# Performance work log

Hardware: AMD Instinct MI355X
Metric: run time of the kernel (lower is better)

The kernel has to match this reference:

```python
import jax, jax.numpy as jnp
import numpy as np

N_NODES = 100000
N_EDGES = 1600000
D = 64
K = 5


def setup_inputs() -> dict:
    key = jax.random.key(0)
    k1, k2, k3, k4 = jax.random.split(key, 4)
    x = jax.random.normal(k1, (N_NODES, D), dtype=jnp.float32)
    # random edges, guaranteed no self-loops (offset in [1, N-1])
    src = jax.random.randint(k2, (N_EDGES,), 0, N_NODES)
    off = jax.random.randint(k3, (N_EDGES,), 1, N_NODES)
    dst = (src + off) % N_NODES
    edge_index = jnp.stack([src, dst], axis=0)  # [2, E], row 0 = source j, row 1 = target i
    kW, kb = jax.random.split(k4)
    W = jax.random.normal(kW, (K, D, D), dtype=jnp.float32) * (1.0 / np.sqrt(D))
    b = jnp.zeros((D,), dtype=jnp.float32)
    return {"x": x, "edge_index": edge_index, "W": W, "b": b}


def reference(x, edge_index, W, b):
    """ChebConv (normalization='sym', lambda_max=2.0) as in PyG GnBlock.

    Scaled Laplacian L_hat = (2/lambda_max) * (I - D^-1/2 A D^-1/2) - I
    with lambda_max=2 has zero diagonal, so propagate(h) = sum over edges
    (j->i) of norm_e * h[j] with norm_e = -dis[j]*dis[i].
    """
    src, dst = edge_index[0], edge_index[1]
    n = x.shape[0]
    # degree over source nodes (PyG get_laplacian scatters edge_weight=1 over row)
    deg = jax.ops.segment_sum(jnp.ones_like(src, dtype=x.dtype), src, num_segments=n)
    dis = jnp.where(deg > 0, jax.lax.rsqrt(jnp.maximum(deg, 1e-30)), 0.0)
    norm = -dis[src] * dis[dst]  # [E]

    def prop(h):
        # message: norm_e * h[src], aggregated at dst
        return jax.ops.segment_sum(norm[:, None] * h[src], dst, num_segments=n)

    Tx0 = x
    out = Tx0 @ W[0]
    Tx1 = prop(x)
    out = out + Tx1 @ W[1]
    for k in range(2, W.shape[0]):
        Tx2 = 2.0 * prop(Tx1) - Tx0
        out = out + Tx2 @ W[k]
        Tx0, Tx1 = Tx1, Tx2
    return out + b
```

## Files before the change

kernel.cpp:

```cpp
#include <hip/hip_runtime.h>

#define DD 64
#define NPB 16
#define NBS 64
#define NBKMAX 128
#define CAPB 20480
#define EPB 8
#define EPT 20

typedef _Float16 f16x8 __attribute__((ext_vector_type(8)));
typedef float f32x4 __attribute__((ext_vector_type(4)));

__global__ __launch_bounds__(1024) void histS_kernel(
        const int* __restrict__ src, unsigned char* __restrict__ srcp,
        int N, int NR, int E, int slice) {
    extern __shared__ unsigned int ldsH[];
    int nw = NR >> 2;
    int t = threadIdx.x;
    for (int i = t; i < nw; i += 1024) ldsH[i] = 0u;
    __syncthreads();
    int base = blockIdx.x * slice;
    int end = min(base + slice, E);
    for (int e = base + t; e < end; e += 1024) {
        int s = __builtin_nontemporal_load(src + e);
        atomicAdd(&ldsH[s >> 2], 1u << ((unsigned int)(s & 3) * 8u));
    }
    __syncthreads();
    unsigned int* outp = reinterpret_cast<unsigned int*>(srcp + (size_t)blockIdx.x * NR);
    for (int i = t; i < nw; i += 1024) outp[i] = ldsH[i];
}

__global__ void disred_kernel(const unsigned char* __restrict__ srcp,
                              float* __restrict__ dis, int N, int NR) {
    int g = blockIdx.x * 256 + threadIdx.x;
    if (g < N) {
        int degv = 0;
        #pragma unroll 8
        for (int i = 0; i < NBS; ++i) degv += srcp[(size_t)i * NR + g];
        dis[g] = (degv > 0) ? rsqrtf((float)degv) : 0.0f;
    }
}

__global__ __launch_bounds__(1024) void histA_kernel(
        const int* __restrict__ src, const int* __restrict__ dst,
        int* __restrict__ gbcnt, unsigned int* __restrict__ bktbuf,
        int E, int nbk) {
    __shared__ int lcnt[NBKMAX];
    __shared__ int lbase[NBKMAX];
    int t = threadIdx.x;
    if (t < NBKMAX) lcnt[t] = 0;
    __syncthreads();
    int base = blockIdx.x * (EPB * 1024);
    unsigned int ent[EPB];
    int rk[EPB];
    int bk[EPB];
    #pragma unroll
    for (int k = 0; k < EPB; ++k) {
        int e = base + t + k * 1024;
        bk[k] = -1;
        if (e < E) {
            int s = __builtin_nontemporal_load(src + e);
            int d = __builtin_nontemporal_load(dst + e);
            int b = d >> 10;
            ent[k] = ((unsigned int)s << 10) | (unsigned int)(d & 1023);
            rk[k] = atomicAdd(&lcnt[b], 1);
            bk[k] = b;
        }
    }
    __syncthreads();
    if (t < nbk) lbase[t] = atomicAdd(&gbcnt[t], lcnt[t]);
    __syncthreads();
    #pragma unroll
    for (int k = 0; k < EPB; ++k) {
        if (bk[k] >= 0) {
            int pos = lbase[bk[k]] + rk[k];
            if (pos < CAPB)
                __builtin_nontemporal_store(ent[k],
                    bktbuf + (size_t)bk[k] * CAPB + pos);
        }
    }
}

__global__ __launch_bounds__(1024) void csrB_kernel(
        const unsigned int* __restrict__ bktbuf, const int* __restrict__ gbcnt,
        int* __restrict__ rowptr, int* __restrict__ adjS,
        int N, int nbk, int E) {
    __shared__ int ncnt[1024];
    __shared__ int tmp[1024];
    __shared__ int adjstage[CAPB];
    __shared__ int bbase_s;
    int b = blockIdx.x;
    int t = threadIdx.x;
    if (t == 0) {
        int acc = 0;
        for (int i = 0; i < b; ++i) acc += gbcnt[i];
        bbase_s = acc;
    }
    ncnt[t] = 0;
    __syncthreads();
    int total = min(gbcnt[b], CAPB);
    int bbase = bbase_s;
    const unsigned int* bp = bktbuf + (size_t)b * CAPB;
    unsigned int sv[EPT];
    int rk[EPT];
    int dl[EPT];
    #pragma unroll
    for (int k = 0; k < EPT; ++k) {
        int i = t + k * 1024;
        dl[k] = -1;
        if (i < total) {
            unsigned int v = bp[i];
            sv[k] = v >> 10;
            int d = (int)(v & 1023u);
            dl[k] = d;
            rk[k] = atomicAdd(&ncnt[d], 1);
        }
    }
    __syncthreads();
    int v = ncnt[t];
    tmp[t] = v;
    __syncthreads();
    for (int off = 1; off < 1024; off <<= 1) {
        int a = (t >= off) ? tmp[t - off] : 0;
        __syncthreads();
        tmp[t] += a;
        __syncthreads();
    }
    int excl = tmp[t] - v;
    int node = b * 1024 + t;
    if (node < N) rowptr[node] = bbase + excl;
    if (b == nbk - 1 && t == 1023) rowptr[N] = E;
    __syncthreads();
    ncnt[t] = excl;
    __syncthreads();
    #pragma unroll
    for (int k = 0; k < EPT; ++k)
        if (dl[k] >= 0) adjstage[ncnt[dl[k]] + rk[k]] = (int)sv[k];
    __syncthreads();
    for (int i = t; i < total; i += 1024)
        adjS[bbase + i] = adjstage[i];
}

__global__ void cvt_kernel(const float* __restrict__ x, const float* __restrict__ dis,
                           _Float16* __restrict__ p0, long long n8) {
    long long i = (long long)blockIdx.x * blockDim.x + threadIdx.x;
    if (i < n8) {
        int node = (int)(i >> 3);
        float dv = dis[node];
        float f = (dv > 0.f) ? dv : 1.0f;
        const float4* x4 = reinterpret_cast<const float4*>(x);
        float4 a = x4[i * 2], b = x4[i * 2 + 1];
        f16x8 h;
        h[0] = (_Float16)(f * a.x); h[1] = (_Float16)(f * a.y);
        h[2] = (_Float16)(f * a.z); h[3] = (_Float16)(f * a.w);
        h[4] = (_Float16)(f * b.x); h[5] = (_Float16)(f * b.y);
        h[6] = (_Float16)(f * b.z); h[7] = (_Float16)(f * b.w);
        reinterpret_cast<f16x8*>(p0)[i] = h;
    }
}

__global__ void wcvt_kernel(const float* __restrict__ W, _Float16* __restrict__ Wh,
                            int nfrag) {
    int idx = blockIdx.x * blockDim.x + threadIdx.x;
    if (idx >= nfrag) return;
    int lane = idx & 63;
    int ct = (idx >> 6) & 3;
    int kt = (idx >> 8) & 1;
    int k = idx >> 9;
    int r0 = kt * 32 + (lane >> 4) * 8;
    int c = ct * 16 + (lane & 15);
    f16x8 h;
    #pragma unroll
    for (int i = 0; i < 8; ++i)
        h[i] = (_Float16)W[(size_t)k * DD * DD + (size_t)(r0 + i) * DD + c];
    reinterpret_cast<f16x8*>(Wh)[idx] = h;
}

__global__ __launch_bounds__(256, 8) void prop_kernel(
        const int* __restrict__ rowptr, const int* __restrict__ adjS,
        const float* __restrict__ dis,
        const _Float16* __restrict__ h, const _Float16* t0,
        _Float16* __restrict__ pout, float scale, int N) {
    int t = threadIdx.x;
    int nl = t >> 6, lane = t & 63;
    int q = lane & 7;
    int s = (lane >> 3) & 1;
    int ng = lane >> 4;
    int node = blockIdx.x * NPB + nl * 4 + ng;
    bool valid = node < N;
    const f16x8* h8 = reinterpret_cast<const f16x8*>(h);

    int beg = 0, end = 0;
    if (valid) { beg = rowptr[node]; end = rowptr[node + 1]; }

    float acc[8];
    #pragma unroll
    for (int i = 0; i < 8; ++i) acc[i] = 0.f;

    int j = beg + s;
    int e0 = (j < end) ? adjS[j] : 0;
    int e1 = (j + 2 < end) ? adjS[j + 2] : 0;
    int e2 = (j + 4 < end) ? adjS[j + 4] : 0;
    int e3 = (j + 6 < end) ? adjS[j + 6] : 0;
    float m0 = (j < end) ? 1.f : 0.f;
    float m1 = (j + 2 < end) ? 1.f : 0.f;
    float m2 = (j + 4 < end) ? 1.f : 0.f;
    float m3 = (j + 6 < end) ? 1.f : 0.f;
    while (j < end) {
        int jn = j + 8;
        int n0 = (jn < end) ? adjS[jn] : 0;
        int n1 = (jn + 2 < end) ? adjS[jn + 2] : 0;
        int n2 = (jn + 4 < end) ? adjS[jn + 4] : 0;
        int n3 = (jn + 6 < end) ? adjS[jn + 6] : 0;
        float nm0 = (jn < end) ? 1.f : 0.f;
        float nm1 = (jn + 2 < end) ? 1.f : 0.f;
        float nm2 = (jn + 4 < end) ? 1.f : 0.f;
        float nm3 = (jn + 6 < end) ? 1.f : 0.f;
        f16x8 g0 = h8[(size_t)e0 * 8 + q];
        f16x8 g1 = h8[(size_t)e1 * 8 + q];
        f16x8 g2 = h8[(size_t)e2 * 8 + q];
        f16x8 g3 = h8[(size_t)e3 * 8 + q];
        #pragma unroll
        for (int i = 0; i < 8; ++i) {
            acc[i] += m0 * (float)g0[i] + m1 * (float)g1[i];
            acc[i] += m2 * (float)g2[i] + m3 * (float)g3[i];
        }
        e0 = n0; e1 = n1; e2 = n2; e3 = n3;
        m0 = nm0; m1 = nm1; m2 = nm2; m3 = nm3;
        j = jn;
    }
    #pragma unroll
    for (int i = 0; i < 8; ++i) acc[i] += __shfl_xor(acc[i], 8, 64);

    if (s == 0 && valid) {
        float dv = dis[node];
        float cf = scale * dv * dv;
        size_t base = (size_t)node * DD + q * 8;
        f16x8 vh;
        if (t0) {
            f16x8 t0v = __builtin_nontemporal_load(
                reinterpret_cast<const f16x8*>(t0 + base));
            #pragma unroll
            for (int i = 0; i < 8; ++i)
                vh[i] = (_Float16)(cf * acc[i] - (float)t0v[i]);
        } else {
            #pragma unroll
            for (int i = 0; i < 8; ++i) vh[i] = (_Float16)(cf * acc[i]);
        }
        *reinterpret_cast<f16x8*>(pout + base) = vh;
    }
}

static __device__ __forceinline__ f16x8 afrag(const _Float16* __restrict__ P,
                                              int node, int kt, int lk) {
    return *reinterpret_cast<const f16x8*>(P + (size_t)node * DD + kt * 32 + lk * 8);
}

__global__ __launch_bounds__(256, 8) void gemm5_kernel(
        const _Float16* __restrict__ P0, const _Float16* __restrict__ P1,
        const _Float16* __restrict__ P2, const _Float16* __restrict__ P3,
        const _Float16* __restrict__ P4,
        const float* __restrict__ dis, const _Float16* __restrict__ Wh,
        const float* __restrict__ bias, float* __restrict__ out, int N) {
    int t = threadIdx.x;
    int nl = t >> 6, lane = t & 63;
    int ct = nl, lr = lane & 15, lk = lane >> 4;
    const f16x8* Wh8 = reinterpret_cast<const f16x8*>(Wh);
    f16x8 bf[5][2];
    #pragma unroll
    for (int k = 0; k < 5; ++k)
        #pragma unroll
        for (int kt = 0; kt < 2; ++kt)
            bf[k][kt] = Wh8[((k * 2 + kt) * 4 + ct) * 64 + lane];
    int col = ct * 16 + lr;
    float bv = bias[col];

    int nb0 = blockIdx.x * NPB;
    if (nb0 >= N) return;
    int node = min(nb0 + lr, N - 1);
    f32x4 d = {0.f, 0.f, 0.f, 0.f};
    #pragma unroll
    for (int kt = 0; kt < 2; ++kt) {
        d = __builtin_amdgcn_mfma_f32_16x16x32_f16(afrag(P0, node, kt, lk), bf[0][kt], d, 0, 0, 0);
        d = __builtin_amdgcn_mfma_f32_16x16x32_f16(afrag(P1, node, kt, lk), bf[1][kt], d, 0, 0, 0);
        d = __builtin_amdgcn_mfma_f32_16x16x32_f16(afrag(P2, node, kt, lk), bf[2][kt], d, 0, 0, 0);
        d = __builtin_amdgcn_mfma_f32_16x16x32_f16(afrag(P3, node, kt, lk), bf[3][kt], d, 0, 0, 0);
        d = __builtin_amdgcn_mfma_f32_16x16x32_f16(afrag(P4, node, kt, lk), bf[4][kt], d, 0, 0, 0);
    }
    int nvb = min(NPB, N - nb0);
    #pragma unroll
    for (int r = 0; r < 4; ++r) {
        int row = lk * 4 + r;
        if (row < nvb) {
            float dv = dis[nb0 + row];
            float invd = (dv > 0.f) ? 1.f / dv : 1.f;
            long long o = (long long)(nb0 + row) * DD + col;
            __builtin_nontemporal_store(bv + invd * d[r], out + o);
        }
    }
}

__global__ __launch_bounds__(256, 8) void gemm2_kernel(
        const _Float16* __restrict__ P0, const _Float16* __restrict__ P1,
        const float* __restrict__ dis,
        const float* __restrict__ W0, const float* __restrict__ W1,
        const float* __restrict__ bias, float* __restrict__ out, int N) {
    int t = threadIdx.x;
    int nl = t >> 6, lane = t & 63;
    int ct = nl, lr = lane & 15, lk = lane >> 4;
    f16x8 bf0[2], bf1[2];
    #pragma unroll
    for (int kt = 0; kt < 2; ++kt)
        #pragma unroll
        for (int i = 0; i < 8; ++i) {
            int r = kt * 32 + lk * 8 + i;
            bf0[kt][i] = (_Float16)W0[r * DD + ct * 16 + lr];
            bf1[kt][i] = (_Float16)W1[r * DD + ct * 16 + lr];
        }
    int nb0 = blockIdx.x * NPB;
    int node = min(nb0 + lr, N - 1);
    f32x4 d = {0.f, 0.f, 0.f, 0.f};
    #pragma unroll
    for (int kt = 0; kt < 2; ++kt) {
        d = __builtin_amdgcn_mfma_f32_16x16x32_f16(afrag(P0, node, kt, lk), bf0[kt], d, 0, 0, 0);
        d = __builtin_amdgcn_mfma_f32_16x16x32_f16(afrag(P1, node, kt, lk), bf1[kt], d, 0, 0, 0);
    }
    int nvb = min(NPB, N - nb0);
    int col = ct * 16 + lr;
    float bv = bias[col];
    #pragma unroll
    for (int r = 0; r < 4; ++r) {
        int row = lk * 4 + r;
        if (row < nvb) {
            float dv = dis[nb0 + row];
            float invd = (dv > 0.f) ? 1.f / dv : 1.f;
            long long o = (long long)(nb0 + row) * DD + col;
            out[o] = bv + invd * d[r];
        }
    }
}

__global__ __launch_bounds__(256, 8) void gemm1_kernel(
        const _Float16* __restrict__ P, const float* __restrict__ dis,
        const float* __restrict__ Wk, float* __restrict__ out, int N) {
    int t = threadIdx.x;
    int nl = t >> 6, lane = t & 63;
    int ct = nl, lr = lane & 15, lk = lane >> 4;
    f16x8 bf[2];
    #pragma unroll
    for (int kt = 0; kt < 2; ++kt)
        #pragma unroll
        for (int i = 0; i < 8; ++i) {
            int r = kt * 32 + lk * 8 + i;
            bf[kt][i] = (_Float16)Wk[r * DD + ct * 16 + lr];
        }
    int nb0 = blockIdx.x * NPB;
    int node = min(nb0 + lr, N - 1);
    f32x4 d = {0.f, 0.f, 0.f, 0.f};
    #pragma unroll
    for (int kt = 0; kt < 2; ++kt)
        d = __builtin_amdgcn_mfma_f32_16x16x32_f16(afrag(P, node, kt, lk), bf[kt], d, 0, 0, 0);
    int nvb = min(NPB, N - nb0);
    int col = ct * 16 + lr;
    #pragma unroll
    for (int r = 0; r < 4; ++r) {
        int row = lk * 4 + r;
        if (row < nvb) {
            float dv = dis[nb0 + row];
            float invd = (dv > 0.f) ? 1.f / dv : 1.f;
            long long o = (long long)(nb0 + row) * DD + col;
            out[o] = out[o] + invd * d[r];
        }
    }
}

extern "C" void kernel_launch(void* const* d_in, const int* in_sizes, int n_in,
                              void* d_out, int out_size, void* d_ws, size_t ws_size,
                              hipStream_t stream) {
    const float* x  = (const float*)d_in[0];
    const int*   ei = (const int*)d_in[1];
    const float* W  = (const float*)d_in[2];
    const float* b  = (const float*)d_in[3];
    float* out = (float*)d_out;

    const int N = in_sizes[0] / DD;
    const int E = in_sizes[1] / 2;
    const int K = in_sizes[2] / (DD * DD);
    const long long ND = (long long)N * DD;
    const int NR = ((N + 3) / 4) * 4;
    const int nbk = (N + 1023) >> 10;

    const int* src = ei;
    const int* dst = ei + E;

    size_t off = 0;
    char* base = (char*)d_ws;
    auto alloc = [&](size_t bytes) {
        char* p = base + off;
        off = (off + bytes + 63) & ~(size_t)63;
        return p;
    };
    float* dis = (float*)alloc((size_t)N * 4);
    int* rowptr = (int*)alloc((size_t)(N + 1) * 4);
    _Float16* Wh = (_Float16*)alloc((size_t)5 * 2 * 4 * 64 * 8 * 2);
    int* gbcnt = (int*)alloc((size_t)NBKMAX * 4);
    char* ovl = alloc((size_t)NBS * NR + (size_t)NBKMAX * CAPB * 4);
    unsigned char* srcp = (unsigned char*)ovl;
    unsigned int* bktbuf = (unsigned int*)(ovl + (size_t)NBS * NR);
    int* adjS = (int*)alloc((size_t)E * 4);
    _Float16* P0 = (_Float16*)alloc((size_t)ND * 2);
    _Float16* P1 = (_Float16*)alloc((size_t)ND * 2);
    _Float16* P3 = (_Float16*)alloc((size_t)ND * 2);
    _Float16* P4 = (_Float16*)alloc((size_t)ND * 2);
    _Float16* P2 = (_Float16*)ovl;

    (void)hipMemsetAsync(gbcnt, 0, (size_t)NBKMAX * 4, stream);

    const int sliceS = (E + NBS - 1) / NBS;
    histS_kernel<<<NBS, 1024, (size_t)NR, stream>>>(src, srcp, N, NR, E, sliceS);
    disred_kernel<<<(N + 255) / 256, 256, 0, stream>>>(srcp, dis, N, NR);

    const int na = (E + EPB * 1024 - 1) / (EPB * 1024);
    histA_kernel<<<na, 1024, 0, stream>>>(src, dst, gbcnt, bktbuf, E, nbk);
    csrB_kernel<<<nbk, 1024, 0, stream>>>(bktbuf, gbcnt, rowptr, adjS, N, nbk, E);

    const long long n8 = ND / 8;
    cvt_kernel<<<(int)((n8 + 255) / 256), 256, 0, stream>>>(x, dis, P0, n8);
    if (K == 5) {
        const int nfrag = 5 * 2 * 4 * 64;
        wcvt_kernel<<<(nfrag + 255) / 256, 256, 0, stream>>>(W, Wh, nfrag);
    }

    const int pgrid = (N + NPB - 1) / NPB;
    const int Wsz = DD * DD;

    if (K == 5) {
        prop_kernel<<<pgrid, 256, 0, stream>>>(rowptr, adjS, dis, P0,
                                               (const _Float16*)0, P1, -1.0f, N);
        prop_kernel<<<pgrid, 256, 0, stream>>>(rowptr, adjS, dis, P1, P0, P2, -2.0f, N);
        prop_kernel<<<pgrid, 256, 0, stream>>>(rowptr, adjS, dis, P2, P1, P3, -2.0f, N);
        prop_kernel<<<pgrid, 256, 0, stream>>>(rowptr, adjS, dis, P3, P2, P4, -2.0f, N);
        gemm5_kernel<<<pgrid, 256, 0, stream>>>(P0, P1, P2, P3, P4, dis, Wh, b, out, N);
    } else {
        prop_kernel<<<pgrid, 256, 0, stream>>>(rowptr, adjS, dis, P0,
                                               (const _Float16*)0, P1, -1.0f, N);
        gemm2_kernel<<<pgrid, 256, 0, stream>>>(P0, P1, dis, W, W + Wsz, b, out, N);
        _Float16* t0 = P0;
        _Float16* h  = P1;
        _Float16* fr = P2;
        for (int k = 2; k < K; ++k) {
            prop_kernel<<<pgrid, 256, 0, stream>>>(rowptr, adjS, dis, h, t0, fr, -2.0f, N);
            gemm1_kernel<<<pgrid, 256, 0, stream>>>(fr, dis, W + (long long)k * Wsz,
                                                    out, N);
            _Float16* nfree = t0;
            t0 = h; h = fr; fr = nfree;
        }
    }
}
```

Before: 333.5 us.

## Fuse degree histogram into bucket pass and final propagation into GEMM

```diff
diff --git a/kernel.cpp b/kernel.cpp
--- a/kernel.cpp
+++ b/kernel.cpp
@@ -2,52 +2,26 @@
 
 #define DD 64
 #define NPB 16
-#define NBS 64
 #define NBKMAX 128
 #define CAPB 20480
 #define EPB 8
 #define EPT 20
+#define ASTR 72
 
 typedef _Float16 f16x8 __attribute__((ext_vector_type(8)));
 typedef float f32x4 __attribute__((ext_vector_type(4)));
 
-__global__ __launch_bounds__(1024) void histS_kernel(
-        const int* __restrict__ src, unsigned char* __restrict__ srcp,
-        int N, int NR, int E, int slice) {
+__global__ __launch_bounds__(1024) void histA_kernel(
+        const int* __restrict__ src, const int* __restrict__ dst,
+        int* __restrict__ gbcnt, unsigned int* __restrict__ bktbuf,
+        unsigned char* __restrict__ srcp, int NR,
+        int E, int nbk) {
     extern __shared__ unsigned int ldsH[];
+    __shared__ int lcnt[NBKMAX];
+    __shared__ int lbase[NBKMAX];
     int nw = NR >> 2;
     int t = threadIdx.x;
     for (int i = t; i < nw; i += 1024) ldsH[i] = 0u;
-    __syncthreads();
-    int base = blockIdx.x * slice;
-    int end = min(base + slice, E);
-    for (int e = base + t; e < end; e += 1024) {
-        int s = __builtin_nontemporal_load(src + e);
-        atomicAdd(&ldsH[s >> 2], 1u << ((unsigned int)(s & 3) * 8u));
-    }
-    __syncthreads();
-    unsigned int* outp = reinterpret_cast<unsigned int*>(srcp + (size_t)blockIdx.x * NR);
-    for (int i = t; i < nw; i += 1024) outp[i] = ldsH[i];
-}
-
-__global__ void disred_kernel(const unsigned char* __restrict__ srcp,
-                              float* __restrict__ dis, int N, int NR) {
-    int g = blockIdx.x * 256 + threadIdx.x;
-    if (g < N) {
-        int degv = 0;
-        #pragma unroll 8
-        for (int i = 0; i < NBS; ++i) degv += srcp[(size_t)i * NR + g];
-        dis[g] = (degv > 0) ? rsqrtf((float)degv) : 0.0f;
-    }
-}
-
-__global__ __launch_bounds__(1024) void histA_kernel(
-        const int* __restrict__ src, const int* __restrict__ dst,
-        int* __restrict__ gbcnt, unsigned int* __restrict__ bktbuf,
-        int E, int nbk) {
-    __shared__ int lcnt[NBKMAX];
-    __shared__ int lbase[NBKMAX];
-    int t = threadIdx.x;
     if (t < NBKMAX) lcnt[t] = 0;
     __syncthreads();
     int base = blockIdx.x * (EPB * 1024);
@@ -61,6 +35,7 @@
         if (e < E) {
             int s = __builtin_nontemporal_load(src + e);
             int d = __builtin_nontemporal_load(dst + e);
+            atomicAdd(&ldsH[s >> 2], 1u << ((unsigned int)(s & 3) * 8u));
             int b = d >> 10;
             ent[k] = ((unsigned int)s << 10) | (unsigned int)(d & 1023);
             rk[k] = atomicAdd(&lcnt[b], 1);
@@ -78,6 +53,18 @@
                 __builtin_nontemporal_store(ent[k],
                     bktbuf + (size_t)bk[k] * CAPB + pos);
         }
+    }
+    unsigned int* outp = reinterpret_cast<unsigned int*>(srcp + (size_t)blockIdx.x * NR);
+    for (int i = t; i < nw; i += 1024) outp[i] = ldsH[i];
+}
+
+__global__ void disred_kernel(const unsigned char* __restrict__ srcp,
+                              float* __restrict__ dis, int N, int NR, int na) {
+    int g = blockIdx.x * 256 + threadIdx.x;
+    if (g < N) {
+        int degv = 0;
+        for (int i = 0; i < na; ++i) degv += srcp[(size_t)i * NR + g];
+        dis[g] = (degv > 0) ? rsqrtf((float)degv) : 0.0f;
     }
 }
 
@@ -256,14 +243,80 @@
     return *reinterpret_cast<const f16x8*>(P + (size_t)node * DD + kt * 32 + lk * 8);
 }
 
-__global__ __launch_bounds__(256, 8) void gemm5_kernel(
+__global__ __launch_bounds__(256, 6) void prop_last_kernel(
+        const int* __restrict__ rowptr, const int* __restrict__ adjS,
+        const float* __restrict__ dis,
+        const _Float16* __restrict__ h , const _Float16* __restrict__ t0 ,
         const _Float16* __restrict__ P0, const _Float16* __restrict__ P1,
-        const _Float16* __restrict__ P2, const _Float16* __restrict__ P3,
-        const _Float16* __restrict__ P4,
-        const float* __restrict__ dis, const _Float16* __restrict__ Wh,
-        const float* __restrict__ bias, float* __restrict__ out, int N) {
+        const _Float16* __restrict__ Wh, const float* __restrict__ bias,
+        float* __restrict__ out, int N) {
+    __shared__ _Float16 A_lds[NPB][ASTR];
     int t = threadIdx.x;
     int nl = t >> 6, lane = t & 63;
+    int q = lane & 7;
+    int s = (lane >> 3) & 1;
+    int ng = lane >> 4;
+    int nb0 = blockIdx.x * NPB;
+    int node = nb0 + nl * 4 + ng;
+    bool valid = node < N;
+    const f16x8* h8 = reinterpret_cast<const f16x8*>(h);
+
+    int beg = 0, end = 0;
+    if (valid) { beg = rowptr[node]; end = rowptr[node + 1]; }
+
+    float acc[8];
+    #pragma unroll
+    for (int i = 0; i < 8; ++i) acc[i] = 0.f;
+
+    int j = beg + s;
+    int e0 = (j < end) ? adjS[j] : 0;
+    int e1 = (j + 2 < end) ? adjS[j + 2] : 0;
+    int e2 = (j + 4 < end) ? adjS[j + 4] : 0;
+    int e3 = (j + 6 < end) ? adjS[j + 6] : 0;
+    float m0 = (j < end) ? 1.f : 0.f;
+    float m1 = (j + 2 < end) ? 1.f : 0.f;
+    float m2 = (j + 4 < end) ? 1.f : 0.f;
+    float m3 = (j + 6 < end) ? 1.f : 0.f;
+    while (j < end) {
+        int jn = j + 8;
+        int n0 = (jn < end) ? adjS[jn] : 0;
+        int n1 = (jn + 2 < end) ? adjS[jn + 2] : 0;
+        int n2 = (jn + 4 < end) ? adjS[jn + 4] : 0;
+        int n3 = (jn + 6 < end) ? adjS[jn + 6] : 0;
+        float nm0 = (jn < end) ? 1.f : 0.f;
+        float nm1 = (jn + 2 < end) ? 1.f : 0.f;
+        float nm2 = (jn + 4 < end) ? 1.f : 0.f;
+        float nm3 = (jn + 6 < end) ? 1.f : 0.f;
+        f16x8 g0 = h8[(size_t)e0 * 8 + q];
+        f16x8 g1 = h8[(size_t)e1 * 8 + q];
+        f16x8 g2 = h8[(size_t)e2 * 8 + q];
+        f16x8 g3 = h8[(size_t)e3 * 8 + q];
+        #pragma unroll
+        for (int i = 0; i < 8; ++i) {
+            acc[i] += m0 * (float)g0[i] + m1 * (float)g1[i];
+            acc[i] += m2 * (float)g2[i] + m3 * (float)g3[i];
+        }
+        e0 = n0; e1 = n1; e2 = n2; e3 = n3;
+        m0 = nm0; m1 = nm1; m2 = nm2; m3 = nm3;
+        j = jn;
+    }
+    #pragma unroll
+    for (int i = 0; i < 8; ++i) acc[i] += __shfl_xor(acc[i], 8, 64);
+
+    if (s == 0 && valid) {
+        float dv = dis[node];
+        float cf = -2.0f * dv * dv;
+        size_t base = (size_t)node * DD + q * 8;
+        f16x8 t0v = __builtin_nontemporal_load(
+            reinterpret_cast<const f16x8*>(t0 + base));
+        f16x8 vh;
+        #pragma unroll
+        for (int i = 0; i < 8; ++i)
+            vh[i] = (_Float16)(cf * acc[i] - (float)t0v[i]);
+        *reinterpret_cast<f16x8*>(&A_lds[nl * 4 + ng][q * 8]) = vh;
+    }
+    __syncthreads();
+
     int ct = nl, lr = lane & 15, lk = lane >> 4;
     const f16x8* Wh8 = reinterpret_cast<const f16x8*>(Wh);
     f16x8 bf[5][2];
@@ -272,22 +325,20 @@
         #pragma unroll
         for (int kt = 0; kt < 2; ++kt)
             bf[k][kt] = Wh8[((k * 2 + kt) * 4 + ct) * 64 + lane];
+    int gn = min(nb0 + lr, N - 1);
+    f32x4 d = {0.f, 0.f, 0.f, 0.f};
+    #pragma unroll
+    for (int kt = 0; kt < 2; ++kt) {
+        f16x8 a4 = *reinterpret_cast<const f16x8*>(&A_lds[lr][kt * 32 + lk * 8]);
+        d = __builtin_amdgcn_mfma_f32_16x16x32_f16(afrag(P0, gn, kt, lk), bf[0][kt], d, 0, 0, 0);
+        d = __builtin_amdgcn_mfma_f32_16x16x32_f16(afrag(P1, gn, kt, lk), bf[1][kt], d, 0, 0, 0);
+        d = __builtin_amdgcn_mfma_f32_16x16x32_f16(afrag(t0, gn, kt, lk), bf[2][kt], d, 0, 0, 0);
+        d = __builtin_amdgcn_mfma_f32_16x16x32_f16(afrag(h,  gn, kt, lk), bf[3][kt], d, 0, 0, 0);
+        d = __builtin_amdgcn_mfma_f32_16x16x32_f16(a4, bf[4][kt], d, 0, 0, 0);
+    }
+    int nvb = min(NPB, N - nb0);
     int col = ct * 16 + lr;
     float bv = bias[col];
-
-    int nb0 = blockIdx.x * NPB;
-    if (nb0 >= N) return;
-    int node = min(nb0 + lr, N - 1);
-    f32x4 d = {0.f, 0.f, 0.f, 0.f};
-    #pragma unroll
-    for (int kt = 0; kt < 2; ++kt) {
-        d = __builtin_amdgcn_mfma_f32_16x16x32_f16(afrag(P0, node, kt, lk), bf[0][kt], d, 0, 0, 0);
-        d = __builtin_amdgcn_mfma_f32_16x16x32_f16(afrag(P1, node, kt, lk), bf[1][kt], d, 0, 0, 0);
-        d = __builtin_amdgcn_mfma_f32_16x16x32_f16(afrag(P2, node, kt, lk), bf[2][kt], d, 0, 0, 0);
-        d = __builtin_amdgcn_mfma_f32_16x16x32_f16(afrag(P3, node, kt, lk), bf[3][kt], d, 0, 0, 0);
-        d = __builtin_amdgcn_mfma_f32_16x16x32_f16(afrag(P4, node, kt, lk), bf[4][kt], d, 0, 0, 0);
-    }
-    int nvb = min(NPB, N - nb0);
     #pragma unroll
     for (int r = 0; r < 4; ++r) {
         int row = lk * 4 + r;
@@ -389,6 +440,7 @@
     const long long ND = (long long)N * DD;
     const int NR = ((N + 3) / 4) * 4;
     const int nbk = (N + 1023) >> 10;
+    const int na = (E + EPB * 1024 - 1) / (EPB * 1024);
 
     const int* src = ei;
     const int* dst = ei + E;
@@ -404,24 +456,20 @@
     int* rowptr = (int*)alloc((size_t)(N + 1) * 4);
     _Float16* Wh = (_Float16*)alloc((size_t)5 * 2 * 4 * 64 * 8 * 2);
     int* gbcnt = (int*)alloc((size_t)NBKMAX * 4);
-    char* ovl = alloc((size_t)NBS * NR + (size_t)NBKMAX * CAPB * 4);
+    char* ovl = alloc((size_t)na * NR + (size_t)NBKMAX * CAPB * 4);
     unsigned char* srcp = (unsigned char*)ovl;
-    unsigned int* bktbuf = (unsigned int*)(ovl + (size_t)NBS * NR);
+    unsigned int* bktbuf = (unsigned int*)(ovl + (size_t)na * NR);
     int* adjS = (int*)alloc((size_t)E * 4);
     _Float16* P0 = (_Float16*)alloc((size_t)ND * 2);
     _Float16* P1 = (_Float16*)alloc((size_t)ND * 2);
     _Float16* P3 = (_Float16*)alloc((size_t)ND * 2);
-    _Float16* P4 = (_Float16*)alloc((size_t)ND * 2);
     _Float16* P2 = (_Float16*)ovl;
 
     (void)hipMemsetAsync(gbcnt, 0, (size_t)NBKMAX * 4, stream);
 
-    const int sliceS = (E + NBS - 1) / NBS;
-    histS_kernel<<<NBS, 1024, (size_t)NR, stream>>>(src, srcp, N, NR, E, sliceS);
-    disred_kernel<<<(N + 255) / 256, 256, 0, stream>>>(srcp, dis, N, NR);
-
-    const int na = (E + EPB * 1024 - 1) / (EPB * 1024);
-    histA_kernel<<<na, 1024, 0, stream>>>(src, dst, gbcnt, bktbuf, E, nbk);
+    histA_kernel<<<na, 1024, (size_t)NR, stream>>>(src, dst, gbcnt, bktbuf,
+                                                   srcp, NR, E, nbk);
+    disred_kernel<<<(N + 255) / 256, 256, 0, stream>>>(srcp, dis, N, NR, na);
     csrB_kernel<<<nbk, 1024, 0, stream>>>(bktbuf, gbcnt, rowptr, adjS, N, nbk, E);
 
     const long long n8 = ND / 8;
@@ -439,8 +487,8 @@
                                                (const _Float16*)0, P1, -1.0f, N);
         prop_kernel<<<pgrid, 256, 0, stream>>>(rowptr, adjS, dis, P1, P0, P2, -2.0f, N);
         prop_kernel<<<pgrid, 256, 0, stream>>>(rowptr, adjS, dis, P2, P1, P3, -2.0f, N);
-        prop_kernel<<<pgrid, 256, 0, stream>>>(rowptr, adjS, dis, P3, P2, P4, -2.0f, N);
-        gemm5_kernel<<<pgrid, 256, 0, stream>>>(P0, P1, P2, P3, P4, dis, Wh, b, out, N);
+        prop_last_kernel<<<pgrid, 256, 0, stream>>>(rowptr, adjS, dis, P3, P2,
+                                                    P0, P1, Wh, b, out, N);
     } else {
         prop_kernel<<<pgrid, 256, 0, stream>>>(rowptr, adjS, dis, P0,
                                                (const _Float16*)0, P1, -1.0f, N);
```

New measurement: 343.3 us. 1.03x slower.
